# Kernel optimization log

Hardware: AMD Instinct MI355X
Metric: run time of the kernel (lower is better)

## Reference

```python
import jax, jax.numpy as jnp
import numpy as np

N = 128
INSTANCES = 64
EMBED_DIM = 256
HIDDEN = 1024
BATCH = 2048


def _kaiming(key, dims):
    # matches custom_kaiming: randn * sqrt(2 / dims[-2])
    return jax.random.normal(key, dims, dtype=jnp.float32) * np.sqrt(2.0 / float(dims[-2])).astype(np.float32)


def setup_inputs() -> dict:
    key = jax.random.key(0)
    k_a, k_el, k_er, k_lin, k_un = jax.random.split(key, 5)
    a = jax.random.randint(k_a, (BATCH, 2), 0, N, dtype=jnp.int64 if jax.config.jax_enable_x64 else jnp.int32)
    return {
        "a": a,
        "embedding_left": _kaiming(k_el, (INSTANCES, N, EMBED_DIM)),
        "embedding_right": _kaiming(k_er, (INSTANCES, N, EMBED_DIM)),
        "linear": _kaiming(k_lin, (INSTANCES, EMBED_DIM, HIDDEN)),
        "unembedding": _kaiming(k_un, (INSTANCES, HIDDEN, N)),
    }


def reference(a, embedding_left, embedding_right, linear, unembedding):
    # one-hot @ embedding == direct gather along the vocab axis (same math, O(1) per lookup)
    a1, a2 = a[:, 0], a[:, 1]
    # [instances, batch, embed] -> [batch, instances, embed]
    x1 = jnp.transpose(jnp.take(embedding_left, a1, axis=1), (1, 0, 2))
    x2 = jnp.transpose(jnp.take(embedding_right, a2, axis=1), (1, 0, 2))
    hidden = jnp.einsum('bie,ieh->bih', x1 + x2, linear)
    out = jnp.einsum('bih,ihn->bin', jax.nn.gelu(hidden, approximate=False), unembedding)
    return out
```

## Files before the change

### kernel.cpp

```cpp
#include <hip/hip_runtime.h>
#include <hip/hip_bf16.h>

typedef __bf16 bf16;
typedef __bf16 bf16x8 __attribute__((ext_vector_type(8)));
typedef __bf16 bf16x4 __attribute__((ext_vector_type(4)));
typedef float  f32x4  __attribute__((ext_vector_type(4)));

#define MFMA16(A,B,C) __builtin_amdgcn_mfma_f32_16x16x32_bf16((A),(B),(C),0,0,0)

constexpr int NI    = 64;
constexpr int NN    = 128;
constexpr int E     = 256;
constexpr int HID   = 1024;
constexpr int BATCH = 2048;
constexpr int BM    = 128;
constexpr int BH    = 64;
constexpr int W1P   = E  + 8;
constexpr int W2P   = BH + 8;
constexpr int HP    = BH + 8;

__device__ __forceinline__ void glds16(const void* g, void* l) {
    __builtin_amdgcn_global_load_lds(
        (const __attribute__((address_space(1))) unsigned int*)g,
        (__attribute__((address_space(3))) unsigned int*)l, 16, 0, 0);
}

__device__ __forceinline__ float fast_gelu(float x) {
    float p = 1.5957691216f * __builtin_fmaf(0.044715f * x * x, x, x);
    return x * __builtin_amdgcn_rcpf(1.0f + __expf(-p));
}

__global__ __launch_bounds__(256) void pack_w1(
    const float* __restrict__ in, bf16* __restrict__ out)
{
    __shared__ __align__(16) bf16 t[64][264];
    const int inst = blockIdx.y;
    const int h0   = blockIdx.x * 64;
    const int tid  = threadIdx.x;
    {
        const int hq = tid & 15;
        const int e0 = tid >> 4;
        const float* ip = in + (size_t)inst * E * HID + h0 + hq * 4;
        #pragma unroll
        for (int it = 0; it < 16; ++it) {
            int e = it * 16 + e0;
            f32x4 v = *(const f32x4*)(ip + (size_t)e * HID);
            #pragma unroll
            for (int k = 0; k < 4; ++k) t[hq * 4 + k][e] = (bf16)v[k];
        }
    }
    __syncthreads();
    bf16* op = out + ((size_t)inst * HID + h0) * E;
    #pragma unroll
    for (int it = 0; it < 8; ++it) {
        int o  = it * 256 + tid;
        int hl = o >> 5, p = o & 31;
        int tt = p ^ (hl & 7);
        bf16x8 v = *(const bf16x8*)&t[hl][tt * 8];
        *(bf16x8*)(op + (size_t)o * 8) = v;
    }
}

__global__ __launch_bounds__(256) void pack_w2(
    const float* __restrict__ in, bf16* __restrict__ out)
{
    __shared__ __align__(16) bf16 t[128][68];
    const int inst = blockIdx.y;
    const int c    = blockIdx.x;
    const int tid  = threadIdx.x;
    {
        const int nq = tid & 31;
        const int h0 = tid >> 5;
        const float* ip = in + ((size_t)inst * HID + c * 64) * NN + nq * 4;
        #pragma unroll
        for (int it = 0; it < 8; ++it) {
            int h = it * 8 + h0;
            f32x4 v = *(const f32x4*)(ip + (size_t)h * NN);
            #pragma unroll
            for (int k = 0; k < 4; ++k) t[nq * 4 + k][h] = (bf16)v[k];
        }
    }
    __syncthreads();
    bf16* ob = out + (size_t)inst * NN * HID + (size_t)c * 64;
    #pragma unroll
    for (int it = 0; it < 4; ++it) {
        int o = it * 256 + tid;
        int n = o >> 3, p = o & 7;
        int tt = p ^ (n & 7);
        int k2 = tt >> 2, qq = tt & 3;
        const bf16* r0 = &t[n][k2 * 32 + qq * 4];
        bf16x4 lo = *(const bf16x4*)r0;
        bf16x4 hi = *(const bf16x4*)(r0 + 16);
        bf16x8 v;
        v[0] = lo[0]; v[1] = lo[1]; v[2] = lo[2]; v[3] = lo[3];
        v[4] = hi[0]; v[5] = hi[1]; v[6] = hi[2]; v[7] = hi[3];
        *(bf16x8*)(ob + (size_t)n * 1024 + p * 8) = v;
    }
}

__global__ __launch_bounds__(256, 3) void mlp3_fused_v2(
    const int*   __restrict__ a,
    const float* __restrict__ embL,
    const float* __restrict__ embR,
    const bf16*  __restrict__ W1,
    const bf16*  __restrict__ W2,
    float* __restrict__ out)
{
    __shared__ __align__(16) bf16 sW1[BH * E];
    __shared__ __align__(16) bf16 sW2[NN * BH];

    const int blk   = blockIdx.x;
    const int xcd   = blk & 7;
    const int j     = blk >> 3;
    const int inst  = xcd + 8 * (j >> 4);
    const int btile = j & 15;

    const int tid  = threadIdx.x;
    const int wave = tid >> 6;
    const int lane = tid & 63;
    const int m  = lane & 15;
    const int q  = lane >> 4;
    const int xm = m & 7;

    bf16x8 aF[2][8];
    #pragma unroll
    for (int rt = 0; rt < 2; ++rt) {
        const int r  = btile * BM + wave * 32 + rt * 16 + m;
        const int i1 = a[2 * r + 0];
        const int i2 = a[2 * r + 1];
        const float* pl = embL + ((size_t)inst * NN + i1) * E;
        const float* pr = embR + ((size_t)inst * NN + i2) * E;
        #pragma unroll
        for (int ks = 0; ks < 8; ++ks) {
            const int e0 = ks * 32 + q * 8;
            f32x4 l0 = *(const f32x4*)(pl + e0);
            f32x4 l1 = *(const f32x4*)(pl + e0 + 4);
            f32x4 r0 = *(const f32x4*)(pr + e0);
            f32x4 r1 = *(const f32x4*)(pr + e0 + 4);
            bf16x8 s;
            #pragma unroll
            for (int k = 0; k < 4; ++k) {
                s[k]     = (bf16)(l0[k] + r0[k]);
                s[k + 4] = (bf16)(l1[k] + r1[k]);
            }
            aF[rt][ks] = s;
        }
    }

    f32x4 O[2][8];
    #pragma unroll
    for (int rt = 0; rt < 2; ++rt)
        #pragma unroll
        for (int ct = 0; ct < 8; ++ct)
            O[rt][ct] = (f32x4){0.f, 0.f, 0.f, 0.f};

    const char* w1g = (const char*)W1 + (size_t)inst * (HID * E * 2);
    const char* w2g = (const char*)W2 + (size_t)inst * (NN * HID * 2);
    char* s1 = (char*)sW1;
    char* s2 = (char*)sW2;

    #pragma unroll 1
    for (int c = 0; c < HID / BH; ++c) {
        __syncthreads();
        {
            const char* g1 = w1g + c * (BH * E * 2);
            #pragma unroll
            for (int it = 0; it < 8; ++it) {
                const int b = it * 4 + wave;
                glds16(g1 + b * 1024 + lane * 16, s1 + b * 1024);
            }
            const char* g2 = w2g + c * 128;
            #pragma unroll
            for (int it = 0; it < 4; ++it) {
                const int b = it * 4 + wave;
                const int n = b * 8 + (lane >> 3);
                glds16(g2 + (size_t)n * 2048 + (lane & 7) * 16, s2 + b * 1024);
            }
        }
        __syncthreads();

        #pragma unroll
        for (int k2 = 0; k2 < 2; ++k2) {
            bf16x8 pa[2];
            #pragma unroll
            for (int cth = 0; cth < 2; ++cth) {
                const int ct = k2 * 2 + cth;
                f32x4 S0 = (f32x4){0.f, 0.f, 0.f, 0.f};
                f32x4 S1 = (f32x4){0.f, 0.f, 0.f, 0.f};
                #pragma unroll
                for (int ks = 0; ks < 8; ++ks) {
                    const int sw = ((ks * 4 + q) ^ xm) * 16;
                    bf16x8 w1f = *(const bf16x8*)(s1 + (ct * 16 + m) * 512 + sw);
                    S0 = MFMA16(w1f, aF[0][ks], S0);
                    S1 = MFMA16(w1f, aF[1][ks], S1);
                }
                #pragma unroll
                for (int rr = 0; rr < 4; ++rr) {
                    pa[0][cth * 4 + rr] = (bf16)fast_gelu(S0[rr]);
                    pa[1][cth * 4 + rr] = (bf16)fast_gelu(S1[rr]);
                }
            }
            #pragma unroll
            for (int ct2 = 0; ct2 < 8; ++ct2) {
                const int sw = ((k2 * 4 + q) ^ xm) * 16;
                bf16x8 w2f = *(const bf16x8*)(s2 + (ct2 * 16 + m) * 128 + sw);
                O[0][ct2] = MFMA16(pa[0], w2f, O[0][ct2]);
                O[1][ct2] = MFMA16(pa[1], w2f, O[1][ct2]);
            }
        }
    }

    #pragma unroll
    for (int rt = 0; rt < 2; ++rt)
        #pragma unroll
        for (int ct = 0; ct < 8; ++ct)
            #pragma unroll
            for (int rr = 0; rr < 4; ++rr) {
                const int b = btile * BM + wave * 32 + rt * 16 + q * 4 + rr;
                const int n = ct * 16 + m;
                out[((size_t)b * NI + inst) * NN + n] = O[rt][ct][rr];
            }
}

__global__ __launch_bounds__(256, 2) void mlp3_fallback(
    const int*   __restrict__ a,
    const float* __restrict__ embL,
    const float* __restrict__ embR,
    const float* __restrict__ W1,
    const float* __restrict__ W2,
    float* __restrict__ out)
{
    __shared__ __align__(16) bf16 sW1[BH][W1P];
    __shared__ __align__(16) bf16 sW2[NN][W2P];
    __shared__ __align__(16) bf16 sH [BM][HP];

    const int blk   = blockIdx.x;
    const int xcd   = blk & 7;
    const int j     = blk >> 3;
    const int inst  = xcd + 8 * (j >> 4);
    const int btile = j & 15;

    const int tid  = threadIdx.x;
    const int wave = tid >> 6;
    const int lane = tid & 63;
    const int m = lane & 15;
    const int q = lane >> 4;

    bf16x8 aF[2][8];
    #pragma unroll
    for (int rt = 0; rt < 2; ++rt) {
        const int r  = btile * BM + wave * 32 + rt * 16 + m;
        const int i1 = a[2 * r + 0];
        const int i2 = a[2 * r + 1];
        const float* pl = embL + ((size_t)inst * NN + i1) * E;
        const float* pr = embR + ((size_t)inst * NN + i2) * E;
        #pragma unroll
        for (int ks = 0; ks < 8; ++ks) {
            const int e0 = ks * 32 + q * 8;
            f32x4 l0 = *(const f32x4*)(pl + e0);
            f32x4 l1 = *(const f32x4*)(pl + e0 + 4);
            f32x4 r0 = *(const f32x4*)(pr + e0);
            f32x4 r1 = *(const f32x4*)(pr + e0 + 4);
            bf16x8 s;
            #pragma unroll
            for (int k = 0; k < 4; ++k) {
                s[k]     = (bf16)(l0[k] + r0[k]);
                s[k + 4] = (bf16)(l1[k] + r1[k]);
            }
            aF[rt][ks] = s;
        }
    }

    f32x4 O[2][8];
    #pragma unroll
    for (int rt = 0; rt < 2; ++rt)
        #pragma unroll
        for (int ct = 0; ct < 8; ++ct)
            O[rt][ct] = (f32x4){0.f, 0.f, 0.f, 0.f};

    #pragma unroll 1
    for (int c = 0; c < HID / BH; ++c) {
        __syncthreads();
        #pragma unroll
        for (int it = 0; it < 8; ++it) {
            const int idx = it * 256 + tid;
            const int e = idx >> 3, h8 = idx & 7;
            f32x4 v0 = *(const f32x4*)(W1 + ((size_t)inst * E + e) * HID + c * BH + h8 * 8);
            f32x4 v1 = *(const f32x4*)(W1 + ((size_t)inst * E + e) * HID + c * BH + h8 * 8 + 4);
            #pragma unroll
            for (int k = 0; k < 4; ++k) {
                sW1[h8 * 8 + k][e]     = (bf16)v0[k];
                sW1[h8 * 8 + k + 4][e] = (bf16)v1[k];
            }
        }
        #pragma unroll
        for (int it = 0; it < 4; ++it) {
            const int idx = it * 256 + tid;
            const int h = idx >> 4, n8 = idx & 15;
            f32x4 v0 = *(const f32x4*)(W2 + ((size_t)inst * HID + c * BH + h) * NN + n8 * 8);
            f32x4 v1 = *(const f32x4*)(W2 + ((size_t)inst * HID + c * BH + h) * NN + n8 * 8 + 4);
            #pragma unroll
            for (int k = 0; k < 4; ++k) {
                sW2[n8 * 8 + k][h]     = (bf16)v0[k];
                sW2[n8 * 8 + k + 4][h] = (bf16)v1[k];
            }
        }
        __syncthreads();

        f32x4 S[2][4];
        #pragma unroll
        for (int rt = 0; rt < 2; ++rt)
            #pragma unroll
            for (int ct = 0; ct < 4; ++ct) S[rt][ct] = (f32x4){0.f, 0.f, 0.f, 0.f};
        #pragma unroll
        for (int ks = 0; ks < 8; ++ks) {
            #pragma unroll
            for (int ct = 0; ct < 4; ++ct) {
                bf16x8 b = *(const bf16x8*)&sW1[ct * 16 + m][ks * 32 + q * 8];
                S[0][ct] = MFMA16(aF[0][ks], b, S[0][ct]);
                S[1][ct] = MFMA16(aF[1][ks], b, S[1][ct]);
            }
        }

        #pragma unroll
        for (int rt = 0; rt < 2; ++rt)
            #pragma unroll
            for (int ct = 0; ct < 4; ++ct)
                #pragma unroll
                for (int rr = 0; rr < 4; ++rr)
                    sH[wave * 32 + rt * 16 + q * 4 + rr][ct * 16 + m] =
                        (bf16)fast_gelu(S[rt][ct][rr]);
        asm volatile("s_waitcnt lgkmcnt(0)" ::: "memory");

        #pragma unroll
        for (int k2 = 0; k2 < 2; ++k2) {
            bf16x8 h0 = *(const bf16x8*)&sH[wave * 32 +  0 + m][k2 * 32 + q * 8];
            bf16x8 h1 = *(const bf16x8*)&sH[wave * 32 + 16 + m][k2 * 32 + q * 8];
            #pragma unroll
            for (int ct = 0; ct < 8; ++ct) {
                bf16x8 b = *(const bf16x8*)&sW2[ct * 16 + m][k2 * 32 + q * 8];
                O[0][ct] = MFMA16(h0, b, O[0][ct]);
                O[1][ct] = MFMA16(h1, b, O[1][ct]);
            }
        }
    }

    #pragma unroll
    for (int rt = 0; rt < 2; ++rt)
        #pragma unroll
        for (int ct = 0; ct < 8; ++ct)
            #pragma unroll
            for (int rr = 0; rr < 4; ++rr) {
                const int b = btile * BM + wave * 32 + rt * 16 + q * 4 + rr;
                const int n = ct * 16 + m;
                out[((size_t)b * NI + inst) * NN + n] = O[rt][ct][rr];
            }
}

extern "C" void kernel_launch(void* const* d_in, const int* in_sizes, int n_in,
                              void* d_out, int out_size, void* d_ws, size_t ws_size,
                              hipStream_t stream)
{
    const int*   a    = (const int*)d_in[0];
    const float* embL = (const float*)d_in[1];
    const float* embR = (const float*)d_in[2];
    const float* lin  = (const float*)d_in[3];
    const float* une  = (const float*)d_in[4];
    float* out = (float*)d_out;

    const size_t w1t_elems = (size_t)NI * HID * E;
    const size_t w2t_elems = (size_t)NI * NN * HID;
    const size_t need = (w1t_elems + w2t_elems) * sizeof(bf16);

    const int nblocks = (BATCH / BM) * NI;

    if (ws_size >= need) {
        bf16* w1t = (bf16*)d_ws;
        bf16* w2t = w1t + w1t_elems;
        pack_w1<<<dim3(HID / 64, NI), 256, 0, stream>>>(lin, w1t);
        pack_w2<<<dim3(HID / BH, NI), 256, 0, stream>>>(une, w2t);
        mlp3_fused_v2<<<nblocks, 256, 0, stream>>>(
            a, embL, embR, w1t, w2t, out);
    } else {
        mlp3_fallback<<<nblocks, 256, 0, stream>>>(
            a, embL, embR, lin, une, out);
    }
}
```

Measured before the change: 325.6 us.

## Prefetch next weight chunk into registers while computing current chunk

Replaces direct global-to-LDS loads, which were issued and then waited on before compute, with a register-staged software pipeline. The next chunk's W1/W2 tiles are loaded into registers during compute on the current chunk, then written to shared memory at the start of the next iteration. This hides global load latency behind MFMA work but adds 12 bf16x8 registers per thread. To make room for them, launch bounds drop from 3 to 2 blocks per SM, which lowers occupancy.

```diff
diff --git a/kernel.cpp b/kernel.cpp
--- a/kernel.cpp
+++ b/kernel.cpp
@@ -18,12 +18,6 @@
 constexpr int W1P   = E  + 8;
 constexpr int W2P   = BH + 8;
 constexpr int HP    = BH + 8;
-
-__device__ __forceinline__ void glds16(const void* g, void* l) {
-    __builtin_amdgcn_global_load_lds(
-        (const __attribute__((address_space(1))) unsigned int*)g,
-        (__attribute__((address_space(3))) unsigned int*)l, 16, 0, 0);
-}
 
 __device__ __forceinline__ float fast_gelu(float x) {
     float p = 1.5957691216f * __builtin_fmaf(0.044715f * x * x, x, x);
@@ -98,7 +92,7 @@
     }
 }
 
-__global__ __launch_bounds__(256, 3) void mlp3_fused_v2(
+__global__ __launch_bounds__(256, 2) void mlp3_fused_v4(
     const int*   __restrict__ a,
     const float* __restrict__ embL,
     const float* __restrict__ embR,
@@ -122,6 +116,29 @@
     const int q  = lane >> 4;
     const int xm = m & 7;
 
+    const char* w1g = (const char*)W1 + (size_t)inst * (HID * E * 2);
+    const char* w2g = (const char*)W2 + (size_t)inst * (NN * HID * 2);
+    char* s1 = (char*)sW1;
+    char* s2 = (char*)sW2;
+
+    bf16x8 rg[12];
+
+    {
+        const char* g1 = w1g;
+        #pragma unroll
+        for (int it = 0; it < 8; ++it) {
+            const int b = it * 4 + wave;
+            rg[it] = *(const bf16x8*)(g1 + b * 1024 + lane * 16);
+        }
+        const char* g2 = w2g;
+        #pragma unroll
+        for (int it = 0; it < 4; ++it) {
+            const int b = it * 4 + wave;
+            const int n = b * 8 + (lane >> 3);
+            rg[8 + it] = *(const bf16x8*)(g2 + (size_t)n * 2048 + (lane & 7) * 16);
+        }
+    }
+
     bf16x8 aF[2][8];
     #pragma unroll
     for (int rt = 0; rt < 2; ++rt) {
@@ -154,30 +171,36 @@
         for (int ct = 0; ct < 8; ++ct)
             O[rt][ct] = (f32x4){0.f, 0.f, 0.f, 0.f};
 
-    const char* w1g = (const char*)W1 + (size_t)inst * (HID * E * 2);
-    const char* w2g = (const char*)W2 + (size_t)inst * (NN * HID * 2);
-    char* s1 = (char*)sW1;
-    char* s2 = (char*)sW2;
-
     #pragma unroll 1
     for (int c = 0; c < HID / BH; ++c) {
         __syncthreads();
-        {
-            const char* g1 = w1g + c * (BH * E * 2);
+        #pragma unroll
+        for (int it = 0; it < 8; ++it) {
+            const int b = it * 4 + wave;
+            *(bf16x8*)(s1 + b * 1024 + lane * 16) = rg[it];
+        }
+        #pragma unroll
+        for (int it = 0; it < 4; ++it) {
+            const int b = it * 4 + wave;
+            *(bf16x8*)(s2 + b * 1024 + lane * 16) = rg[8 + it];
+        }
+        __syncthreads();
+
+        if (c + 1 < HID / BH) {
+            const char* g1 = w1g + (size_t)(c + 1) * (BH * E * 2);
             #pragma unroll
             for (int it = 0; it < 8; ++it) {
                 const int b = it * 4 + wave;
-                glds16(g1 + b * 1024 + lane * 16, s1 + b * 1024);
-            }
-            const char* g2 = w2g + c * 128;
+                rg[it] = *(const bf16x8*)(g1 + b * 1024 + lane * 16);
+            }
+            const char* g2 = w2g + (size_t)(c + 1) * 128;
             #pragma unroll
             for (int it = 0; it < 4; ++it) {
                 const int b = it * 4 + wave;
                 const int n = b * 8 + (lane >> 3);
-                glds16(g2 + (size_t)n * 2048 + (lane & 7) * 16, s2 + b * 1024);
-            }
-        }
-        __syncthreads();
+                rg[8 + it] = *(const bf16x8*)(g2 + (size_t)n * 2048 + (lane & 7) * 16);
+            }
+        }
 
         #pragma unroll
         for (int k2 = 0; k2 < 2; ++k2) {
@@ -378,8 +401,8 @@
         bf16* w1t = (bf16*)d_ws;
         bf16* w2t = w1t + w1t_elems;
         pack_w1<<<dim3(HID / 64, NI), 256, 0, stream>>>(lin, w1t);
-        pack_w2<<<dim3(HID / BH, NI), 256, 0, stream>>>(une, w2t);
-        mlp3_fused_v2<<<nblocks, 256, 0, stream>>>(
+        pack_w2<<<dim3(HID / 64, NI), 256, 0, stream>>>(une, w2t);
+        mlp3_fused_v4<<<nblocks, 256, 0, stream>>>(
             a, embL, embR, w1t, w2t, out);
     } else {
         mlp3_fallback<<<nblocks, 256, 0, stream>>>(
```

Measured after the change: 300.4 us. 7.7% less time.
